# Performance work log

Hardware: AMD Instinct MI355X
Metric: run time of the kernel (lower is better)

## Reference

```python
import jax, jax.numpy as jnp
import numpy as np

B, N, D = 32, 65536, 16
M, H, OUT = 32, 64, 3  # m_model_output, hidden width, i_model output


def setup_inputs() -> dict:
    key = jax.random.key(0)
    ks = jax.random.split(key, 5)
    s = lambda fan_in: 1.0 / np.sqrt(fan_in)
    return {
        "inputs": jax.random.normal(ks[0], (B, N, D), dtype=jnp.float32),
        "mw1": jax.random.normal(ks[1], (D, H), dtype=jnp.float32) * s(D),
        "mb1": jnp.zeros((H,), dtype=jnp.float32),
        "mw2": jax.random.normal(ks[2], (H, M), dtype=jnp.float32) * s(H),
        "mb2": jnp.zeros((M,), dtype=jnp.float32),
        "iw1": jax.random.normal(ks[3], (M + 1, H), dtype=jnp.float32) * s(M + 1),
        "ib1": jnp.zeros((H,), dtype=jnp.float32),
        "iw2": jax.random.normal(ks[4], (H, OUT), dtype=jnp.float32) * s(H),
        "ib2": jnp.zeros((OUT,), dtype=jnp.float32),
    }


def reference(inputs, mw1, mb1, mw2, mb2, iw1, ib1, iw2, ib2):
    # m_model: per-node MLP producing messages [B, N, M]
    h = jax.nn.relu(jnp.einsum("bnd,dh->bnh", inputs, mw1) + mb1)
    messages = jnp.einsum("bnh,hm->bnm", h, mw2) + mb2
    # concat(messages[:j], messages[j:]) is identity -> sum over ALL nodes
    msg_sum = jnp.sum(messages, axis=1, keepdims=True)  # [B, 1, M]
    msg_sum = jnp.broadcast_to(msg_sum, (inputs.shape[0], inputs.shape[1], messages.shape[-1]))
    # append each node's last scalar feature -> [B, N, M+1]
    feat = jnp.concatenate([msg_sum, inputs[..., -1:]], axis=-1)
    # i_model: per-node MLP -> [B, N, OUT]
    g = jax.nn.relu(jnp.einsum("bnf,fh->bnh", feat, iw1) + ib1)
    out = jnp.einsum("bnh,ho->bno", g, iw2) + ib2
    return out
```

## Files before the change

kernel.cpp:

```cpp
#include <hip/hip_runtime.h>

#define Bb   32
#define Nn   65536
#define Dd   16
#define Hh   64
#define Mm   32
#define OUTn 3

#define NPW   256
#define WPB_N (Nn / NPW)
#define TPB   256

typedef __attribute__((ext_vector_type(8)))  __bf16 bf16x8;
typedef __attribute__((ext_vector_type(16))) float  f32x16;
typedef __attribute__((ext_vector_type(4)))  float  f32x4;

static __device__ inline void split_bf(float w, __bf16& hi, __bf16& lo) {
    hi = (__bf16)w;
    lo = (__bf16)(w - (float)hi);
}

__global__ __launch_bounds__(TPB) void k_mphase(
    const float* __restrict__ in, const float* __restrict__ mw1,
    const float* __restrict__ mb1, float* __restrict__ partials,
    float* __restrict__ xlast)
{
    const int lane = threadIdx.x & 63;
    const int l31  = lane & 31;
    const int half = lane >> 5;
    const int wid  = blockIdx.x * (TPB / 64) + (threadIdx.x >> 6);
    const size_t node0 = (size_t)wid * NPW;

    bf16x8 bhiA, bloA, bhiB, bloB;
#pragma unroll
    for (int e = 0; e < 8; ++e) {
        const int k = 8 * half + e;
        __bf16 h, l;
        split_bf(mw1[k * Hh + l31], h, l);        bhiA[e] = h; bloA[e] = l;
        split_bf(mw1[k * Hh + 32 + l31], h, l);   bhiB[e] = h; bloB[e] = l;
    }
    const float biasA = mb1[l31];
    const float biasB = mb1[32 + l31];

    float hsumA = 0.f, hsumB = 0.f;
    const float* __restrict__ inw = in + node0 * Dd;

    for (int s = 0; s < NPW / 32; ++s) {
        const float* ap = inw + ((size_t)(s * 32 + l31)) * Dd + 8 * half;
        f32x4 v0 = *(const f32x4*)ap;
        f32x4 v1 = *(const f32x4*)(ap + 4);
        bf16x8 a;
        a[0] = (__bf16)v0[0]; a[1] = (__bf16)v0[1];
        a[2] = (__bf16)v0[2]; a[3] = (__bf16)v0[3];
        a[4] = (__bf16)v1[0]; a[5] = (__bf16)v1[1];
        a[6] = (__bf16)v1[2]; a[7] = (__bf16)v1[3];

        f32x16 accA, accB;
#pragma unroll
        for (int r = 0; r < 16; ++r) { accA[r] = biasA; accB[r] = biasB; }
        accA = __builtin_amdgcn_mfma_f32_32x32x16_bf16(a, bloA, accA, 0, 0, 0);
        accA = __builtin_amdgcn_mfma_f32_32x32x16_bf16(a, bhiA, accA, 0, 0, 0);
        accB = __builtin_amdgcn_mfma_f32_32x32x16_bf16(a, bloB, accB, 0, 0, 0);
        accB = __builtin_amdgcn_mfma_f32_32x32x16_bf16(a, bhiB, accB, 0, 0, 0);

        float mA[16], mB[16];
#pragma unroll
        for (int r = 0; r < 16; ++r) {
            mA[r] = fmaxf(accA[r], 0.f);
            mB[r] = fmaxf(accB[r], 0.f);
        }
#pragma unroll
        for (int st = 8; st >= 1; st >>= 1)
#pragma unroll
            for (int r = 0; r < st; ++r) { mA[r] += mA[r + st]; mB[r] += mB[r + st]; }
        hsumA += mA[0]; hsumB += mB[0];

        float x15 = __shfl_xor(v1[3], 32, 64);
        if (lane < 32) xlast[node0 + (size_t)s * 32 + lane] = x15;
    }

    hsumA += __shfl_xor(hsumA, 32, 64);
    hsumB += __shfl_xor(hsumB, 32, 64);
    partials[(size_t)wid * Hh + lane] = (lane < 32) ? hsumA : hsumB;
}

__global__ void k_combine(const float* __restrict__ partials,
                          const float* __restrict__ mw2, const float* __restrict__ mb2,
                          const float* __restrict__ iw1, const float* __restrict__ ib1,
                          float* __restrict__ base)
{
    const int b = blockIdx.x;
    const int t = threadIdx.x;
    float hs = 0.f;
    for (int c = 0; c < WPB_N; ++c)
        hs += partials[((size_t)b * WPB_N + c) * Hh + t];
    __shared__ float Hs[Hh];
    __shared__ float ms[Mm];
    Hs[t] = hs;
    __syncthreads();
    if (t < Mm) {
        float s = (float)Nn * mb2[t];
        for (int h = 0; h < Hh; ++h) s = fmaf(Hs[h], mw2[h * Mm + t], s);
        ms[t] = s;
    }
    __syncthreads();
    float bs = ib1[t];
    for (int m = 0; m < Mm; ++m) bs = fmaf(ms[m], iw1[m * Hh + t], bs);
    base[(size_t)b * Hh + t] = bs;
}

__global__ __launch_bounds__(TPB) void k_iphase(
    const float* __restrict__ xsrc, int xstride,
    const float* __restrict__ base,
    const float* __restrict__ iw1, const float* __restrict__ iw2,
    const float* __restrict__ ib2, float* __restrict__ out)
{
    const size_t blk0 = (size_t)blockIdx.x * TPB;
    const int b = (int)(blk0 / Nn);
    const size_t idx = blk0 + threadIdx.x;

    const float x = xsrc[idx * xstride + (xstride - 1)];
    const float* bb  = base + (size_t)b * Hh;
    const float* w1l = iw1 + (size_t)Mm * Hh;

    float o0 = ib2[0], o1 = ib2[1], o2 = ib2[2];
#pragma unroll 16
    for (int h = 0; h < Hh; ++h) {
        float g = fmaxf(fmaf(x, w1l[h], bb[h]), 0.f);
        o0 = fmaf(g, iw2[h * OUTn + 0], o0);
        o1 = fmaf(g, iw2[h * OUTn + 1], o1);
        o2 = fmaf(g, iw2[h * OUTn + 2], o2);
    }
    out[idx * 3 + 0] = o0;
    out[idx * 3 + 1] = o1;
    out[idx * 3 + 2] = o2;
}

extern "C" void kernel_launch(void* const* d_in, const int* in_sizes, int n_in,
                              void* d_out, int out_size, void* d_ws, size_t ws_size,
                              hipStream_t stream) {
    const float* in  = (const float*)d_in[0];
    const float* mw1 = (const float*)d_in[1];
    const float* mb1 = (const float*)d_in[2];
    const float* mw2 = (const float*)d_in[3];
    const float* mb2 = (const float*)d_in[4];
    const float* iw1 = (const float*)d_in[5];
    const float* ib1 = (const float*)d_in[6];
    const float* iw2 = (const float*)d_in[7];
    const float* ib2 = (const float*)d_in[8];
    float* out = (float*)d_out;

    char* ws = (char*)d_ws;
    const size_t PART_SZ = (size_t)Bb * WPB_N * Hh * sizeof(float);
    float* partials = (float*)(ws);
    float* base     = (float*)(ws + PART_SZ);
    float* xlast    = (float*)(ws + PART_SZ + 8192);
    const size_t need = PART_SZ + 8192 + (size_t)Bb * Nn * sizeof(float);
    const int use_xlast = (ws_size >= need) ? 1 : 0;

    const int nwaves  = (Bb * Nn) / NPW;
    const int nblocks = nwaves / (TPB / 64);

    hipLaunchKernelGGL(k_mphase, dim3(nblocks), dim3(TPB), 0, stream,
                       in, mw1, mb1, partials, xlast);
    hipLaunchKernelGGL(k_combine, dim3(Bb), dim3(Hh), 0, stream,
                       partials, mw2, mb2, iw1, ib1, base);
    hipLaunchKernelGGL(k_iphase, dim3((Bb * Nn) / TPB), dim3(TPB), 0, stream,
                       use_xlast ? xlast : in, use_xlast ? 1 : Dd,
                       base, iw1, iw2, ib2, out);
}
```

Measured before the change: 59.53 us.

## Replace per-node i_model MLP with precomputed piecewise-linear segment lookup

Within a batch, every node's i_model input differs only in the scalar last feature. That makes the output a piecewise-linear function of x with up to 64 ReLU knots. The combine kernel now sorts these knots and precomputes slope and intercept per segment, and the i-phase does a binary search plus three FMAs per node instead of a 64-wide MLP. The last-feature buffer is also stored as bf16 to halve its traffic, and per-wave partial sums are replaced by atomicAdd into a memset buffer. The bf16 storage of x adds precision loss, and the knot handling can introduce edge-case error.

New measurement: 64.70 us. 1.09x slower.

```diff
diff --git a/kernel.cpp b/kernel.cpp
--- a/kernel.cpp
+++ b/kernel.cpp
@@ -1,4 +1,5 @@
 #include <hip/hip_runtime.h>
+#include <hip/hip_bf16.h>
 
 #define Bb   32
 #define Nn   65536
@@ -8,10 +9,11 @@
 #define OUTn 3
 
 #define NPW   256
-#define WPB_N (Nn / NPW)
 #define TPB   256
+#define NSEG  65
 
 typedef __attribute__((ext_vector_type(8)))  __bf16 bf16x8;
+typedef __attribute__((ext_vector_type(4)))  __bf16 bf16x4;
 typedef __attribute__((ext_vector_type(16))) float  f32x16;
 typedef __attribute__((ext_vector_type(4)))  float  f32x4;
 
@@ -22,14 +24,15 @@
 
 __global__ __launch_bounds__(TPB) void k_mphase(
     const float* __restrict__ in, const float* __restrict__ mw1,
-    const float* __restrict__ mb1, float* __restrict__ partials,
-    float* __restrict__ xlast)
+    const float* __restrict__ mb1, float* __restrict__ Hsum,
+    __bf16* __restrict__ xlast)
 {
     const int lane = threadIdx.x & 63;
     const int l31  = lane & 31;
     const int half = lane >> 5;
     const int wid  = blockIdx.x * (TPB / 64) + (threadIdx.x >> 6);
     const size_t node0 = (size_t)wid * NPW;
+    const int b = wid >> 8;
 
     bf16x8 bhiA, bloA, bhiB, bloB;
 #pragma unroll
@@ -76,64 +79,113 @@
         hsumA += mA[0]; hsumB += mB[0];
 
         float x15 = __shfl_xor(v1[3], 32, 64);
-        if (lane < 32) xlast[node0 + (size_t)s * 32 + lane] = x15;
+        if (lane < 32) xlast[node0 + (size_t)s * 32 + lane] = (__bf16)x15;
     }
 
     hsumA += __shfl_xor(hsumA, 32, 64);
     hsumB += __shfl_xor(hsumB, 32, 64);
-    partials[(size_t)wid * Hh + lane] = (lane < 32) ? hsumA : hsumB;
-}
-
-__global__ void k_combine(const float* __restrict__ partials,
+    atomicAdd(Hsum + (size_t)b * Hh + lane, (lane < 32) ? hsumA : hsumB);
+}
+
+__global__ void k_combine(const float* __restrict__ Hsum,
                           const float* __restrict__ mw2, const float* __restrict__ mb2,
                           const float* __restrict__ iw1, const float* __restrict__ ib1,
-                          float* __restrict__ base)
+                          const float* __restrict__ iw2, const float* __restrict__ ib2,
+                          float* __restrict__ knotsG, float* __restrict__ segG)
 {
+    __shared__ float sHs[Hh], sMs[Mm], sBase[Hh], sW[Hh], sKn[Hh], sSort[Hh];
+    __shared__ float sIw2[Hh * OUTn];
     const int b = blockIdx.x;
     const int t = threadIdx.x;
-    float hs = 0.f;
-    for (int c = 0; c < WPB_N; ++c)
-        hs += partials[((size_t)b * WPB_N + c) * Hh + t];
-    __shared__ float Hs[Hh];
-    __shared__ float ms[Mm];
-    Hs[t] = hs;
-    __syncthreads();
+
+    if (t < Hh) sHs[t] = Hsum[(size_t)b * Hh + t];
+    for (int i = t; i < Hh * OUTn; i += 128) sIw2[i] = iw2[i];
+    __syncthreads();
+
     if (t < Mm) {
         float s = (float)Nn * mb2[t];
-        for (int h = 0; h < Hh; ++h) s = fmaf(Hs[h], mw2[h * Mm + t], s);
-        ms[t] = s;
-    }
-    __syncthreads();
-    float bs = ib1[t];
-    for (int m = 0; m < Mm; ++m) bs = fmaf(ms[m], iw1[m * Hh + t], bs);
-    base[(size_t)b * Hh + t] = bs;
+        for (int h = 0; h < Hh; ++h) s = fmaf(sHs[h], mw2[h * Mm + t], s);
+        sMs[t] = s;
+    }
+    __syncthreads();
+
+    if (t < Hh) {
+        float bs = ib1[t];
+        for (int m = 0; m < Mm; ++m) bs = fmaf(sMs[m], iw1[m * Hh + t], bs);
+        float w = iw1[Mm * Hh + t];
+        sBase[t] = bs; sW[t] = w;
+        float k = (w != 0.f) ? (-bs / w) : 1e15f;
+        if (!(fabsf(k) < 1e15f)) k = 1e15f;
+        sKn[t] = k;
+    }
+    __syncthreads();
+
+    if (t < Hh) {
+        float k = sKn[t];
+        int r = 0;
+        for (int j = 0; j < Hh; ++j) {
+            float kj = sKn[j];
+            r += (kj < k || (kj == k && j < t)) ? 1 : 0;
+        }
+        sSort[r] = k;
+    }
+    __syncthreads();
+
+    if (t < Hh) knotsG[(size_t)b * Hh + t] = sSort[t];
+    if (t < NSEG) {
+        float lo = (t == 0)  ? sSort[0] - 1.0f      : sSort[t - 1];
+        float hi = (t == Hh) ? sSort[Hh - 1] + 1.0f : sSort[t];
+        float m  = 0.5f * lo + 0.5f * hi;
+        float A0 = ib2[0], A1 = ib2[1], A2 = ib2[2], B0 = 0.f, B1 = 0.f, B2 = 0.f;
+        for (int h = 0; h < Hh; ++h) {
+            float bs = sBase[h], w = sW[h];
+            if (fmaf(w, m, bs) > 0.f) {
+                A0 = fmaf(bs, sIw2[h * 3 + 0], A0);
+                A1 = fmaf(bs, sIw2[h * 3 + 1], A1);
+                A2 = fmaf(bs, sIw2[h * 3 + 2], A2);
+                B0 = fmaf(w,  sIw2[h * 3 + 0], B0);
+                B1 = fmaf(w,  sIw2[h * 3 + 1], B1);
+                B2 = fmaf(w,  sIw2[h * 3 + 2], B2);
+            }
+        }
+        float* sg = segG + (size_t)b * 6 * NSEG;
+        sg[0 * NSEG + t] = A0; sg[1 * NSEG + t] = A1; sg[2 * NSEG + t] = A2;
+        sg[3 * NSEG + t] = B0; sg[4 * NSEG + t] = B1; sg[5 * NSEG + t] = B2;
+    }
 }
 
 __global__ __launch_bounds__(TPB) void k_iphase(
-    const float* __restrict__ xsrc, int xstride,
-    const float* __restrict__ base,
-    const float* __restrict__ iw1, const float* __restrict__ iw2,
-    const float* __restrict__ ib2, float* __restrict__ out)
+    const __bf16* __restrict__ xl, const float* __restrict__ knotsG,
+    const float* __restrict__ segG, float* __restrict__ out)
 {
-    const size_t blk0 = (size_t)blockIdx.x * TPB;
-    const int b = (int)(blk0 / Nn);
-    const size_t idx = blk0 + threadIdx.x;
-
-    const float x = xsrc[idx * xstride + (xstride - 1)];
-    const float* bb  = base + (size_t)b * Hh;
-    const float* w1l = iw1 + (size_t)Mm * Hh;
-
-    float o0 = ib2[0], o1 = ib2[1], o2 = ib2[2];
-#pragma unroll 16
-    for (int h = 0; h < Hh; ++h) {
-        float g = fmaxf(fmaf(x, w1l[h], bb[h]), 0.f);
-        o0 = fmaf(g, iw2[h * OUTn + 0], o0);
-        o1 = fmaf(g, iw2[h * OUTn + 1], o1);
-        o2 = fmaf(g, iw2[h * OUTn + 2], o2);
-    }
-    out[idx * 3 + 0] = o0;
-    out[idx * 3 + 1] = o1;
-    out[idx * 3 + 2] = o2;
+    __shared__ __align__(16) float sK[Hh];
+    __shared__ float sT[6 * NSEG];
+    const int t = threadIdx.x;
+    const int b = blockIdx.x >> 6;
+
+    if (t < Hh) sK[t] = knotsG[(size_t)b * Hh + t];
+    for (int i = t; i < 6 * NSEG; i += TPB) sT[i] = segG[(size_t)b * 6 * NSEG + i];
+    __syncthreads();
+
+    const size_t n0 = ((size_t)blockIdx.x * TPB + t) * 4;
+    bf16x4 xv = *(const bf16x4*)(xl + n0);
+    float o[12];
+#pragma unroll
+    for (int i = 0; i < 4; ++i) {
+        const float x = (float)xv[i];
+        int pos = 0;
+#pragma unroll
+        for (int st = 32; st >= 1; st >>= 1)
+            pos += (sK[pos + st - 1] < x) ? st : 0;
+        pos += (sK[pos] < x) ? 1 : 0;
+        o[3 * i + 0] = fmaf(sT[3 * NSEG + pos], x, sT[0 * NSEG + pos]);
+        o[3 * i + 1] = fmaf(sT[4 * NSEG + pos], x, sT[1 * NSEG + pos]);
+        o[3 * i + 2] = fmaf(sT[5 * NSEG + pos], x, sT[2 * NSEG + pos]);
+    }
+    f32x4* po = (f32x4*)(out + n0 * 3);
+    po[0] = f32x4{o[0], o[1], o[2],  o[3]};
+    po[1] = f32x4{o[4], o[5], o[6],  o[7]};
+    po[2] = f32x4{o[8], o[9], o[10], o[11]};
 }
 
 extern "C" void kernel_launch(void* const* d_in, const int* in_sizes, int n_in,
@@ -151,21 +203,18 @@
     float* out = (float*)d_out;
 
     char* ws = (char*)d_ws;
-    const size_t PART_SZ = (size_t)Bb * WPB_N * Hh * sizeof(float);
-    float* partials = (float*)(ws);
-    float* base     = (float*)(ws + PART_SZ);
-    float* xlast    = (float*)(ws + PART_SZ + 8192);
-    const size_t need = PART_SZ + 8192 + (size_t)Bb * Nn * sizeof(float);
-    const int use_xlast = (ws_size >= need) ? 1 : 0;
-
-    const int nwaves  = (Bb * Nn) / NPW;
-    const int nblocks = nwaves / (TPB / 64);
-
+    float*  Hsum   = (float*)(ws);
+    float*  knotsG = (float*)(ws + 8192);
+    float*  segG   = (float*)(ws + 16384);
+    __bf16* xl     = (__bf16*)(ws + 131072);
+
+    hipMemsetAsync(Hsum, 0, (size_t)Bb * Hh * sizeof(float), stream);
+
+    const int nblocks = (Bb * Nn / NPW) / (TPB / 64);
     hipLaunchKernelGGL(k_mphase, dim3(nblocks), dim3(TPB), 0, stream,
-                       in, mw1, mb1, partials, xlast);
-    hipLaunchKernelGGL(k_combine, dim3(Bb), dim3(Hh), 0, stream,
-                       partials, mw2, mb2, iw1, ib1, base);
-    hipLaunchKernelGGL(k_iphase, dim3((Bb * Nn) / TPB), dim3(TPB), 0, stream,
-                       use_xlast ? xlast : in, use_xlast ? 1 : Dd,
-                       base, iw1, iw2, ib2, out);
-}
+                       in, mw1, mb1, Hsum, xl);
+    hipLaunchKernelGGL(k_combine, dim3(Bb), dim3(128), 0, stream,
+                       Hsum, mw2, mb2, iw1, ib1, iw2, ib2, knotsG, segG);
+    hipLaunchKernelGGL(k_iphase, dim3((Bb * Nn) / (TPB * 4)), dim3(TPB), 0, stream,
+                       xl, knotsG, segG, out);
+}
```
